# Performance work log

Measured on AMD Instinct MI355X. Metric: run time of the kernel, lower is better.

Reference implementation:

```python
import jax, jax.numpy as jnp
import numpy as np

# Dims: batch N, in_channels C (>=75 so the 0.25/0.75 channel weighting is active),
# prototypes O, 3x3 kernel, 56x56 feature map.
N, C, H, W = 32, 150, 56, 56
O = 225
KH = KW = 3
K = KH * KW
D = C * K  # unfolded feature dim = 1350
SPLIT = 75  # weight_cdist: channels [:75] weight 0.25, [75:] weight 0.75


def setup_inputs() -> dict:
    key = jax.random.key(0)
    k1, k2 = jax.random.split(key)
    x = jax.random.uniform(k1, (N, C, H, W), dtype=jnp.float32)
    # kaiming_uniform_ on a (O, D) matrix: bound = sqrt(6 / fan_in), fan_in = D
    bound = float(np.sqrt(6.0 / D))
    weight = jax.random.uniform(k2, (O, D), jnp.float32, -bound, bound)
    return {"x": x, "weight": weight}


def reference(x, weight):
    n = x.shape[0]
    # im2col, channel-major feature ordering (c, kh, kw) -- matches torch F.unfold
    patches = jax.lax.conv_general_dilated_patches(
        x, (KH, KW), (1, 1), ((1, 1), (1, 1)))  # (N, C*K, H, W)
    windows = patches.reshape(n, D, H * W).transpose(0, 2, 1)  # (N, L, D)
    # per-channel weights, repeated over the K kernel positions
    w = jnp.where(jnp.arange(C) < SPLIT, 0.25, 0.75).astype(x.dtype)
    wfull = jnp.repeat(w, K)  # (D,)
    # weighted squared distance: sum_d wfull_d * (x_d - p_d)^2
    #   = ||x||_w^2 + ||p||_w^2 - 2 * x . (w * p)   (GEMM form, no NxOxLxD tensor)
    x2 = jnp.einsum('nld,d->nl', windows * windows, wfull)          # (N, L)
    p2 = jnp.einsum('od,d->o', weight * weight, wfull)              # (O,)
    xp = jnp.einsum('nld,od->nlo', windows, weight * wfull)         # (N, L, O)
    d2 = x2[:, :, None] + p2[None, None, :] - 2.0 * xp
    dist = jnp.sqrt(jnp.maximum(d2, 1e-12))  # clamp tiny negative GEMM round-off
    # (N, L, O) -> (N, O, H, W)
    return dist.transpose(0, 2, 1).reshape(n, O, H, W)
```

## Files before the change

### kernel.cpp

```cpp
#include <hip/hip_runtime.h>

#define N_B   32
#define C_IN  150
#define HH    56
#define WW    56
#define O_P   225
#define D_F   1350
#define SPLIT 75

#define C_PAD 160
#define O_PAD 256
#define PSTR  176
#define NPLANE 58
#define PLSZ  (NPLANE * PSTR)

#define SW    2540.0f
#define SC_I  (1.0f / 322580.0f)

typedef __attribute__((ext_vector_type(4))) int int4v;
typedef __attribute__((ext_vector_type(16))) int i32x16;
typedef unsigned char u8;
typedef unsigned int uint_t;

#define XT_OFF 0
#define WT_OFF 16056320
#define AO_OFF (WT_OFF + 368640)
#define SQ_OFF (AO_OFF + 1024)

#define TIDX(c, w) ((c) * 57 + ((c) >> 4) + (w))

__global__ __launch_bounds__(256) void prep_x(const float* __restrict__ x,
                                              u8* __restrict__ xt,
                                              float* __restrict__ sq) {
  __shared__ float tile[150 * 57 + 9 + 56 + 1];
  __shared__ float sp[4][WW];
  const int n = blockIdx.y, h = blockIdx.x, tid = threadIdx.x;

  for (int idx = tid; idx < C_IN * 14; idx += 256) {
    int c = idx / 14, w4 = (idx % 14) * 4;
    const float4 v = *(const float4*)(&x[((size_t)(n * C_IN + c) * HH + h) * WW + w4]);
    tile[TIDX(c, w4 + 0)] = v.x;
    tile[TIDX(c, w4 + 1)] = v.y;
    tile[TIDX(c, w4 + 2)] = v.z;
    tile[TIDX(c, w4 + 3)] = v.w;
  }
  __syncthreads();

  uint4* xt128 = (uint4*)(xt + (size_t)((n * HH + h) * WW) * C_PAD);
  for (int idx = tid; idx < WW * (C_PAD / 16); idx += 256) {
    int w = idx / (C_PAD / 16), q = idx % (C_PAD / 16), c0 = q * 16;
    uint_t words[4];
#pragma unroll
    for (int wd = 0; wd < 4; ++wd) {
      uint_t a = 0;
#pragma unroll
      for (int b = 0; b < 4; ++b) {
        int c = c0 + wd * 4 + b;
        int v = -127;
        if (c < C_IN) v = __float2int_rn(tile[TIDX(c, w)] * 254.f) - 127;
        a |= ((uint_t)(u8)(char)v) << (8 * b);
      }
      words[wd] = a;
    }
    xt128[idx] = make_uint4(words[0], words[1], words[2], words[3]);
  }

  if (tid < 224) {
    int w = tid >> 2, p = tid & 3;
    int cb = p * 38, ce = min(cb + 38, C_IN);
    float s = 0.f;
    for (int c = cb; c < ce; ++c) {
      float v = tile[TIDX(c, w)];
      s += ((c < SPLIT) ? 0.25f : 0.75f) * v * v;
    }
    sp[p][w] = s;
  }
  __syncthreads();
  if (tid < WW)
    sq[(n * HH + h) * WW + tid] = sp[0][tid] + sp[1][tid] + sp[2][tid] + sp[3][tid];
}

__global__ __launch_bounds__(256) void prep_w(const float* __restrict__ wgt,
                                              u8* __restrict__ wt,
                                              float* __restrict__ ao) {
  const int o = blockIdx.x, tid = threadIdx.x;
  const int wv2 = o >> 6, j2 = (o >> 5) & 1, ol = o & 31;

  for (int idx = tid; idx < 9 * C_PAD; idx += 256) {
    int t = idx / C_PAD, c = idx % C_PAD;
    int v = 0;
    if (o < O_P && c < C_IN) {
      float wc = (c < SPLIT) ? 0.25f : 0.75f;
      float f = wgt[o * D_F + c * 9 + t] * wc * SW;
      v = __float2int_rn(fminf(fmaxf(f, -127.f), 127.f));
    }
    int kc = c >> 5, hi2 = (c >> 4) & 1, b = c & 15;
    wt[(size_t)wv2 * 92160 + (t * 5 + kc) * 2048 + j2 * 1024 + hi2 * 512 + ol * 16 + b] =
        (u8)(char)v;
  }

  float s1 = 0.f, s2 = 0.f;
  if (o < O_P)
    for (int d = tid; d < D_F; d += 256) {
      int c = d / 9;
      float wc = (c < SPLIT) ? 0.25f : 0.75f;
      float f = wgt[o * D_F + d] * wc * SW;
      float wq = (float)__float2int_rn(fminf(fmaxf(f, -127.f), 127.f));
      s1 += wq;
      s2 += wq * wq * ((c < SPLIT) ? 4.0f : (4.0f / 3.0f));
    }
  __shared__ float r1[256], r2[256];
  r1[tid] = s1; r2[tid] = s2;
  __syncthreads();
  for (int off = 128; off > 0; off >>= 1) {
    if (tid < off) { r1[tid] += r1[tid + off]; r2[tid] += r2[tid + off]; }
    __syncthreads();
  }
  if (tid == 0) ao[o] = r2[0] / (SW * SW) - r1[0] / SW;
}

__global__ __launch_bounds__(512, 4) void sfm_main(
    const u8* __restrict__ xt, const u8* __restrict__ wt,
    const float* __restrict__ aog, const float* __restrict__ sqg,
    float* __restrict__ out) {
  __shared__ __align__(16) u8 xtile[3 * PLSZ];
  __shared__ float aos[O_PAD];
  __shared__ float sqs[3][NPLANE];
  __shared__ float x2row[64];

  const int bid0 = blockIdx.y * 56 + blockIdx.x;
  const int bid = (bid0 & 7) * 224 + (bid0 >> 3);
  const int h0 = bid % HH, n = bid / HH;
  const int tid = threadIdx.x, lane = tid & 63, wv = tid >> 6;
  const int l31 = lane & 31, hi = lane >> 5;

  for (int idx = tid; idx < 3 * WW * 10; idx += 512) {
    int dh = idx / (WW * 10), rem = idx % (WW * 10);
    int w = rem / 10, q = rem % 10;
    int hh = h0 + dh - 1;
    uint4 v = make_uint4(0x81818181u, 0x81818181u, 0x81818181u, 0x81818181u);
    if (hh >= 0 && hh < HH)
      v = *(const uint4*)(xt + ((size_t)((n * HH + hh) * WW + w) * C_PAD + q * 16));
    *(uint4*)(&xtile[(size_t)dh * PLSZ + (w + 1) * PSTR + q * 16]) = v;
  }
  for (int idx = tid; idx < 60; idx += 512) {
    int dh = idx / 20, r = idx % 20, side = r / 10, q = r % 10;
    int pos = side ? 57 : 0;
    *(uint4*)(&xtile[(size_t)dh * PLSZ + pos * PSTR + q * 16]) =
        make_uint4(0x81818181u, 0x81818181u, 0x81818181u, 0x81818181u);
  }
  for (int idx = tid; idx < 3 * NPLANE; idx += 512) {
    int dh = idx / NPLANE, col = idx % NPLANE;
    int hh = h0 + dh - 1, w = col - 1;
    float v = 0.f;
    if (hh >= 0 && hh < HH && w >= 0 && w < WW) v = sqg[(n * HH + hh) * WW + w];
    sqs[dh][col] = v;
  }
  if (tid < O_PAD) aos[tid] = (tid < O_P) ? aog[tid] : 0.f;
  __syncthreads();

  if (tid < 64) {
    float s = 0.f;
    if (tid < WW) {
#pragma unroll
      for (int a = 0; a < 3; ++a)
        s += sqs[a][tid] + sqs[a][tid + 1] + sqs[a][tid + 2];
    }
    x2row[tid] = s;
  }
  __syncthreads();

  int vb[2][3];
#pragma unroll
  for (int i = 0; i < 2; ++i)
#pragma unroll
    for (int d = 0; d < 3; ++d)
      vb[i][d] = min(i * 32 + l31 + d, 57) * PSTR + hi * 16;

  const int wvs = __builtin_amdgcn_readfirstlane(wv);
  const u8* abase = wt + (size_t)(wvs >> 1) * 92160 + (wvs & 1) * 1024 +
                    hi * 512 + l31 * 16;

  const i32x16 z = {0, 0, 0, 0, 0, 0, 0, 0, 0, 0, 0, 0, 0, 0, 0, 0};
  i32x16 acc[2] = {z, z};

#pragma unroll
  for (int t = 0; t < 9; ++t) {
    const int dh = t / 3, dwo = t % 3;
    const u8* a0 = abase + t * 10240;
    const u8* b0 = &xtile[dh * PLSZ + vb[0][dwo]];
    const u8* b1 = &xtile[dh * PLSZ + vb[1][dwo]];
#pragma unroll
    for (int kc = 0; kc < 5; ++kc) {
      int4v af  = *(const int4v*)(a0 + kc * 2048);
      int4v bf0 = *(const int4v*)(b0 + kc * 32);
      int4v bf1 = *(const int4v*)(b1 + kc * 32);
      acc[0] = __builtin_amdgcn_mfma_i32_32x32x32_i8(af, bf0, acc[0], 0, 0, 0);
      acc[1] = __builtin_amdgcn_mfma_i32_32x32x32_i8(af, bf1, acc[1], 0, 0, 0);
    }
  }

  const int ob = wv * 32 + hi * 4;
#pragma unroll
  for (int ip = 0; ip < 2; ++ip) {
    const int w = ip * 32 + l31;
    if (w < WW) {
      const float x2v = x2row[w];
#pragma unroll
      for (int rg = 0; rg < 16; ++rg) {
        const int o = ob + (rg & 3) + 8 * (rg >> 2);
        if (o < O_P) {
          float d2 = x2v + aos[o] - SC_I * (float)acc[ip][rg];
          out[((size_t)(n * O_P + o) * HH + h0) * WW + w] = sqrtf(fmaxf(d2, 1e-12f));
        }
      }
    }
  }
}

extern "C" void kernel_launch(void* const* d_in, const int* in_sizes, int n_in,
                              void* d_out, int out_size, void* d_ws, size_t ws_size,
                              hipStream_t stream) {
  const float* x      = (const float*)d_in[0];
  const float* weight = (const float*)d_in[1];
  float* out = (float*)d_out;
  char* ws = (char*)d_ws;

  u8* xt = (u8*)(ws + XT_OFF);
  u8* wt = (u8*)(ws + WT_OFF);
  float* ao = (float*)(ws + AO_OFF);
  float* sq = (float*)(ws + SQ_OFF);

  prep_x<<<dim3(HH, N_B), 256, 0, stream>>>(x, xt, sq);
  prep_w<<<dim3(O_PAD), 256, 0, stream>>>(weight, wt, ao);
  sfm_main<<<dim3(56, N_B), 512, 0, stream>>>(xt, wt, ao, sq, out);
}
```

Baseline: 204.7 us.

## Process two output rows per block, fuse prep kernels, prefetch weight fragments

The main GEMM kernel now computes two output rows per block. It loads four input planes and reuses each weight fragment across four MFMAs instead of two, which halves global weight traffic per output and the block count. Weight fragments are software-prefetched four steps ahead in registers. The two prep kernels are merged into one launch, and the weight path stages its row through shared memory first. The trade-offs are more accumulator registers and more LDS per block, which may lower occupancy.

```diff
diff --git a/kernel.cpp b/kernel.cpp
--- a/kernel.cpp
+++ b/kernel.cpp
@@ -29,112 +29,122 @@
 
 #define TIDX(c, w) ((c) * 57 + ((c) >> 4) + (w))
 
-__global__ __launch_bounds__(256) void prep_x(const float* __restrict__ x,
-                                              u8* __restrict__ xt,
-                                              float* __restrict__ sq) {
+__global__ __launch_bounds__(256) void prep_fused(const float* __restrict__ x,
+                                                  const float* __restrict__ wgt,
+                                                  u8* __restrict__ xt,
+                                                  float* __restrict__ sq,
+                                                  u8* __restrict__ wt,
+                                                  float* __restrict__ ao) {
   __shared__ float tile[150 * 57 + 9 + 56 + 1];
   __shared__ float sp[4][WW];
-  const int n = blockIdx.y, h = blockIdx.x, tid = threadIdx.x;
-
-  for (int idx = tid; idx < C_IN * 14; idx += 256) {
-    int c = idx / 14, w4 = (idx % 14) * 4;
-    const float4 v = *(const float4*)(&x[((size_t)(n * C_IN + c) * HH + h) * WW + w4]);
-    tile[TIDX(c, w4 + 0)] = v.x;
-    tile[TIDX(c, w4 + 1)] = v.y;
-    tile[TIDX(c, w4 + 2)] = v.z;
-    tile[TIDX(c, w4 + 3)] = v.w;
-  }
-  __syncthreads();
-
-  uint4* xt128 = (uint4*)(xt + (size_t)((n * HH + h) * WW) * C_PAD);
-  for (int idx = tid; idx < WW * (C_PAD / 16); idx += 256) {
-    int w = idx / (C_PAD / 16), q = idx % (C_PAD / 16), c0 = q * 16;
-    uint_t words[4];
-#pragma unroll
-    for (int wd = 0; wd < 4; ++wd) {
-      uint_t a = 0;
-#pragma unroll
-      for (int b = 0; b < 4; ++b) {
-        int c = c0 + wd * 4 + b;
-        int v = -127;
-        if (c < C_IN) v = __float2int_rn(tile[TIDX(c, w)] * 254.f) - 127;
-        a |= ((uint_t)(u8)(char)v) << (8 * b);
-      }
-      words[wd] = a;
-    }
-    xt128[idx] = make_uint4(words[0], words[1], words[2], words[3]);
-  }
-
-  if (tid < 224) {
-    int w = tid >> 2, p = tid & 3;
-    int cb = p * 38, ce = min(cb + 38, C_IN);
-    float s = 0.f;
-    for (int c = cb; c < ce; ++c) {
-      float v = tile[TIDX(c, w)];
-      s += ((c < SPLIT) ? 0.25f : 0.75f) * v * v;
-    }
-    sp[p][w] = s;
-  }
-  __syncthreads();
-  if (tid < WW)
-    sq[(n * HH + h) * WW + tid] = sp[0][tid] + sp[1][tid] + sp[2][tid] + sp[3][tid];
-}
-
-__global__ __launch_bounds__(256) void prep_w(const float* __restrict__ wgt,
-                                              u8* __restrict__ wt,
-                                              float* __restrict__ ao) {
-  const int o = blockIdx.x, tid = threadIdx.x;
-  const int wv2 = o >> 6, j2 = (o >> 5) & 1, ol = o & 31;
-
-  for (int idx = tid; idx < 9 * C_PAD; idx += 256) {
-    int t = idx / C_PAD, c = idx % C_PAD;
-    int v = 0;
-    if (o < O_P && c < C_IN) {
-      float wc = (c < SPLIT) ? 0.25f : 0.75f;
-      float f = wgt[o * D_F + c * 9 + t] * wc * SW;
-      v = __float2int_rn(fminf(fmaxf(f, -127.f), 127.f));
-    }
-    int kc = c >> 5, hi2 = (c >> 4) & 1, b = c & 15;
-    wt[(size_t)wv2 * 92160 + (t * 5 + kc) * 2048 + j2 * 1024 + hi2 * 512 + ol * 16 + b] =
-        (u8)(char)v;
-  }
-
-  float s1 = 0.f, s2 = 0.f;
-  if (o < O_P)
-    for (int d = tid; d < D_F; d += 256) {
-      int c = d / 9;
-      float wc = (c < SPLIT) ? 0.25f : 0.75f;
-      float f = wgt[o * D_F + d] * wc * SW;
-      float wq = (float)__float2int_rn(fminf(fmaxf(f, -127.f), 127.f));
-      s1 += wq;
-      s2 += wq * wq * ((c < SPLIT) ? 4.0f : (4.0f / 3.0f));
-    }
-  __shared__ float r1[256], r2[256];
-  r1[tid] = s1; r2[tid] = s2;
-  __syncthreads();
-  for (int off = 128; off > 0; off >>= 1) {
-    if (tid < off) { r1[tid] += r1[tid + off]; r2[tid] += r2[tid + off]; }
-    __syncthreads();
-  }
-  if (tid == 0) ao[o] = r2[0] / (SW * SW) - r1[0] / SW;
+  const int b = blockIdx.x, tid = threadIdx.x;
+
+  if (b < N_B * HH) {
+    const int n = b / HH, h = b % HH;
+
+    for (int idx = tid; idx < C_IN * 14; idx += 256) {
+      int c = idx / 14, w4 = (idx % 14) * 4;
+      const float4 v = *(const float4*)(&x[((size_t)(n * C_IN + c) * HH + h) * WW + w4]);
+      tile[TIDX(c, w4 + 0)] = v.x;
+      tile[TIDX(c, w4 + 1)] = v.y;
+      tile[TIDX(c, w4 + 2)] = v.z;
+      tile[TIDX(c, w4 + 3)] = v.w;
+    }
+    __syncthreads();
+
+    uint4* xt128 = (uint4*)(xt + (size_t)((n * HH + h) * WW) * C_PAD);
+    for (int idx = tid; idx < WW * (C_PAD / 16); idx += 256) {
+      int w = idx / (C_PAD / 16), q = idx % (C_PAD / 16), c0 = q * 16;
+      uint_t words[4];
+#pragma unroll
+      for (int wd = 0; wd < 4; ++wd) {
+        uint_t a = 0;
+#pragma unroll
+        for (int bb = 0; bb < 4; ++bb) {
+          int c = c0 + wd * 4 + bb;
+          int v = -127;
+          if (c < C_IN) v = __float2int_rn(tile[TIDX(c, w)] * 254.f) - 127;
+          a |= ((uint_t)(u8)(char)v) << (8 * bb);
+        }
+        words[wd] = a;
+      }
+      xt128[idx] = make_uint4(words[0], words[1], words[2], words[3]);
+    }
+
+    if (tid < 224) {
+      int w = tid >> 2, p = tid & 3;
+      int cb = p * 38, ce = min(cb + 38, C_IN);
+      float s = 0.f;
+      for (int c = cb; c < ce; ++c) {
+        float v = tile[TIDX(c, w)];
+        s += ((c < SPLIT) ? 0.25f : 0.75f) * v * v;
+      }
+      sp[p][w] = s;
+    }
+    __syncthreads();
+    if (tid < WW)
+      sq[(n * HH + h) * WW + tid] = sp[0][tid] + sp[1][tid] + sp[2][tid] + sp[3][tid];
+
+  } else {
+    const int o = b - N_B * HH;
+    const int wv2 = o >> 6, j2 = (o >> 5) & 1, ol = o & 31;
+    float* wrow = tile;
+    float* r1 = tile + 1408;
+    float* r2 = tile + 1664;
+
+    if (o < O_P)
+      for (int d = tid; d < D_F; d += 256) wrow[d] = wgt[o * D_F + d];
+    __syncthreads();
+
+    for (int idx = tid; idx < 9 * C_PAD; idx += 256) {
+      int t = idx / C_PAD, c = idx % C_PAD;
+      int v = 0;
+      if (o < O_P && c < C_IN) {
+        float wc = (c < SPLIT) ? 0.25f : 0.75f;
+        float f = wrow[c * 9 + t] * wc * SW;
+        v = __float2int_rn(fminf(fmaxf(f, -127.f), 127.f));
+      }
+      int kc = c >> 5, hi2 = (c >> 4) & 1, bb = c & 15;
+      wt[(size_t)wv2 * 92160 + (t * 5 + kc) * 2048 + j2 * 1024 + hi2 * 512 + ol * 16 + bb] =
+          (u8)(char)v;
+    }
+
+    float s1 = 0.f, s2 = 0.f;
+    if (o < O_P)
+      for (int d = tid; d < D_F; d += 256) {
+        int c = d / 9;
+        float wc = (c < SPLIT) ? 0.25f : 0.75f;
+        float f = wrow[d] * wc * SW;
+        float wq = (float)__float2int_rn(fminf(fmaxf(f, -127.f), 127.f));
+        s1 += wq;
+        s2 += wq * wq * ((c < SPLIT) ? 4.0f : (4.0f / 3.0f));
+      }
+    r1[tid] = s1; r2[tid] = s2;
+    __syncthreads();
+    for (int off = 128; off > 0; off >>= 1) {
+      if (tid < off) { r1[tid] += r1[tid + off]; r2[tid] += r2[tid + off]; }
+      __syncthreads();
+    }
+    if (tid == 0) ao[o] = r2[0] / (SW * SW) - r1[0] / SW;
+  }
 }
 
 __global__ __launch_bounds__(512, 4) void sfm_main(
     const u8* __restrict__ xt, const u8* __restrict__ wt,
     const float* __restrict__ aog, const float* __restrict__ sqg,
     float* __restrict__ out) {
-  __shared__ __align__(16) u8 xtile[3 * PLSZ];
+  __shared__ __align__(16) u8 xtile[4 * PLSZ];
   __shared__ float aos[O_PAD];
-  __shared__ float sqs[3][NPLANE];
-  __shared__ float x2row[64];
-
-  const int bid0 = blockIdx.y * 56 + blockIdx.x;
-  const int bid = (bid0 & 7) * 224 + (bid0 >> 3);
-  const int h0 = bid % HH, n = bid / HH;
+  __shared__ float sqs[4][NPLANE];
+  __shared__ float x2row[2][64];
+
+  const int bid0 = blockIdx.y * 28 + blockIdx.x;
+  const int bid = (bid0 & 7) * 112 + (bid0 >> 3);
+  const int n = bid / 28, h0 = (bid % 28) * 2;
   const int tid = threadIdx.x, lane = tid & 63, wv = tid >> 6;
   const int l31 = lane & 31, hi = lane >> 5;
 
-  for (int idx = tid; idx < 3 * WW * 10; idx += 512) {
+  for (int idx = tid; idx < 4 * WW * 10; idx += 512) {
     int dh = idx / (WW * 10), rem = idx % (WW * 10);
     int w = rem / 10, q = rem % 10;
     int hh = h0 + dh - 1;
@@ -143,13 +153,13 @@
       v = *(const uint4*)(xt + ((size_t)((n * HH + hh) * WW + w) * C_PAD + q * 16));
     *(uint4*)(&xtile[(size_t)dh * PLSZ + (w + 1) * PSTR + q * 16]) = v;
   }
-  for (int idx = tid; idx < 60; idx += 512) {
+  for (int idx = tid; idx < 80; idx += 512) {
     int dh = idx / 20, r = idx % 20, side = r / 10, q = r % 10;
     int pos = side ? 57 : 0;
     *(uint4*)(&xtile[(size_t)dh * PLSZ + pos * PSTR + q * 16]) =
         make_uint4(0x81818181u, 0x81818181u, 0x81818181u, 0x81818181u);
   }
-  for (int idx = tid; idx < 3 * NPLANE; idx += 512) {
+  for (int idx = tid; idx < 4 * NPLANE; idx += 512) {
     int dh = idx / NPLANE, col = idx % NPLANE;
     int hh = h0 + dh - 1, w = col - 1;
     float v = 0.f;
@@ -159,14 +169,15 @@
   if (tid < O_PAD) aos[tid] = (tid < O_P) ? aog[tid] : 0.f;
   __syncthreads();
 
-  if (tid < 64) {
+  if (tid < 128) {
+    int r = tid >> 6, w = tid & 63;
     float s = 0.f;
-    if (tid < WW) {
+    if (w < WW) {
 #pragma unroll
       for (int a = 0; a < 3; ++a)
-        s += sqs[a][tid] + sqs[a][tid + 1] + sqs[a][tid + 2];
-    }
-    x2row[tid] = s;
+        s += sqs[r + a][w] + sqs[r + a][w + 1] + sqs[r + a][w + 2];
+    }
+    x2row[r][w] = s;
   }
   __syncthreads();
 
@@ -182,36 +193,45 @@
                     hi * 512 + l31 * 16;
 
   const i32x16 z = {0, 0, 0, 0, 0, 0, 0, 0, 0, 0, 0, 0, 0, 0, 0, 0};
-  i32x16 acc[2] = {z, z};
-
-#pragma unroll
-  for (int t = 0; t < 9; ++t) {
+  i32x16 acc00 = z, acc01 = z, acc10 = z, acc11 = z;
+
+  int4v afp[4];
+#pragma unroll
+  for (int d = 0; d < 4; ++d) afp[d] = *(const int4v*)(abase + d * 2048);
+
+#pragma unroll
+  for (int s = 0; s < 45; ++s) {
+    const int4v af = afp[s & 3];
+    if (s + 4 < 45) afp[s & 3] = *(const int4v*)(abase + (s + 4) * 2048);
+    const int t = s / 5, kc = s % 5;
     const int dh = t / 3, dwo = t % 3;
-    const u8* a0 = abase + t * 10240;
-    const u8* b0 = &xtile[dh * PLSZ + vb[0][dwo]];
-    const u8* b1 = &xtile[dh * PLSZ + vb[1][dwo]];
-#pragma unroll
-    for (int kc = 0; kc < 5; ++kc) {
-      int4v af  = *(const int4v*)(a0 + kc * 2048);
-      int4v bf0 = *(const int4v*)(b0 + kc * 32);
-      int4v bf1 = *(const int4v*)(b1 + kc * 32);
-      acc[0] = __builtin_amdgcn_mfma_i32_32x32x32_i8(af, bf0, acc[0], 0, 0, 0);
-      acc[1] = __builtin_amdgcn_mfma_i32_32x32x32_i8(af, bf1, acc[1], 0, 0, 0);
-    }
+    const int4v bf00 = *(const int4v*)(&xtile[(dh + 0) * PLSZ + vb[0][dwo] + kc * 32]);
+    const int4v bf01 = *(const int4v*)(&xtile[(dh + 0) * PLSZ + vb[1][dwo] + kc * 32]);
+    const int4v bf10 = *(const int4v*)(&xtile[(dh + 1) * PLSZ + vb[0][dwo] + kc * 32]);
+    const int4v bf11 = *(const int4v*)(&xtile[(dh + 1) * PLSZ + vb[1][dwo] + kc * 32]);
+    acc00 = __builtin_amdgcn_mfma_i32_32x32x32_i8(af, bf00, acc00, 0, 0, 0);
+    acc01 = __builtin_amdgcn_mfma_i32_32x32x32_i8(af, bf01, acc01, 0, 0, 0);
+    acc10 = __builtin_amdgcn_mfma_i32_32x32x32_i8(af, bf10, acc10, 0, 0, 0);
+    acc11 = __builtin_amdgcn_mfma_i32_32x32x32_i8(af, bf11, acc11, 0, 0, 0);
   }
 
   const int ob = wv * 32 + hi * 4;
 #pragma unroll
-  for (int ip = 0; ip < 2; ++ip) {
-    const int w = ip * 32 + l31;
-    if (w < WW) {
-      const float x2v = x2row[w];
-#pragma unroll
-      for (int rg = 0; rg < 16; ++rg) {
-        const int o = ob + (rg & 3) + 8 * (rg >> 2);
-        if (o < O_P) {
-          float d2 = x2v + aos[o] - SC_I * (float)acc[ip][rg];
-          out[((size_t)(n * O_P + o) * HH + h0) * WW + w] = sqrtf(fmaxf(d2, 1e-12f));
+  for (int r = 0; r < 2; ++r) {
+#pragma unroll
+    for (int ip = 0; ip < 2; ++ip) {
+      const i32x16 a = r ? (ip ? acc11 : acc10) : (ip ? acc01 : acc00);
+      const int w = ip * 32 + l31;
+      if (w < WW) {
+        const float x2v = x2row[r][w];
+#pragma unroll
+        for (int rg = 0; rg < 16; ++rg) {
+          const int o = ob + (rg & 3) + 8 * (rg >> 2);
+          if (o < O_P) {
+            float d2 = x2v + aos[o] - SC_I * (float)a[rg];
+            out[((size_t)(n * O_P + o) * HH + (h0 + r)) * WW + w] =
+                sqrtf(fmaxf(d2, 1e-12f));
+          }
         }
       }
     }
@@ -231,7 +251,6 @@
   float* ao = (float*)(ws + AO_OFF);
   float* sq = (float*)(ws + SQ_OFF);
 
-  prep_x<<<dim3(HH, N_B), 256, 0, stream>>>(x, xt, sq);
-  prep_w<<<dim3(O_PAD), 256, 0, stream>>>(weight, wt, ao);
-  sfm_main<<<dim3(56, N_B), 512, 0, stream>>>(xt, wt, ao, sq, out);
+  prep_fused<<<dim3(N_B * HH + O_PAD), 256, 0, stream>>>(x, weight, xt, sq, wt, ao);
+  sfm_main<<<dim3(28, N_B), 512, 0, stream>>>(xt, wt, ao, sq, out);
 }
```

Result: slower. 304.0 us (+48.5%).
